# Performance work log

Measured on AMD Instinct MI355X. Metric: run time of the kernel, lower is better.

## Reference

```python
import jax, jax.numpy as jnp
import numpy as np
from functools import partial

ALPHA = 0.5
GAMMA = 0.01
BIG = 1e8  # boundary init, matches compute_softdtw (exp(-BIG/gamma)==0)


def pairwise_sq(x, y):
    # x: [N, d], y: [M, d] -> squared euclidean distances [N, M], clamped at 0
    xn = jnp.sum(x * x, axis=1)[:, None]
    yn = jnp.sum(y * y, axis=1)[None, :]
    d = xn + yn - 2.0 * (x @ y.T)
    return jnp.clip(d, 0.0, None)


def softdtw(D, gamma):
    # soft-DTW DP: V[i,j] = D[i-1,j-1] + softmin(V[i,j-1], V[i-1,j-1], V[i-1,j])
    # scan over rows; inner scan over columns (sequential dependence on V[i,j-1])
    N, M = D.shape

    def row_step(prev_row, d_row):
        # prev_row: V[i-1, 0..M]  (length M+1)
        def col_step(v_left, inp):
            d, v_diag, v_up = inp
            r = jnp.stack([v_left, v_diag, v_up]) * (-1.0 / gamma)
            v = d - gamma * jax.nn.logsumexp(r)  # stable soft-min
            return v, v

        _, row_vals = jax.lax.scan(
            col_step,
            jnp.asarray(BIG, D.dtype),                 # V[i, 0]
            (d_row, prev_row[:-1], prev_row[1:]),      # D[i-1,j-1], V[i-1,j-1], V[i-1,j]
        )
        new_row = jnp.concatenate([jnp.full((1,), BIG, D.dtype), row_vals])
        return new_row, None

    init_row = jnp.concatenate(
        [jnp.zeros((1,), D.dtype), jnp.full((M,), BIG, D.dtype)]
    )  # V[0, :] row with V[0,0]=0
    last_row, _ = jax.lax.scan(row_step, init_row, D)
    return last_row[-1]  # V[N, M]


def dilate_loss(y_pred, y_true, alpha=ALPHA, gamma=GAMMA):
    B, N = y_pred.shape[0], y_pred.shape[1]
    t = y_true.reshape(B, -1, 1)
    o = y_pred.reshape(B, -1, 1)
    D = jax.vmap(pairwise_sq)(t, o)  # [B, N, N]

    sd = partial(softdtw, gamma=gamma)
    # shape term: mean soft-DTW value over batch (SoftDTWBatch)
    loss_shape = jnp.mean(jax.vmap(sd)(D))
    # temporal term: E = d softDTW / d D (soft path), mean over batch (PathDTWBatch)
    path = jnp.mean(jax.vmap(jax.grad(sd))(D), axis=0)  # [N, N]
    idx = jnp.arange(1, N + 1, dtype=y_pred.dtype)
    omega = (idx[:, None] - idx[None, :]) ** 2  # pairwise_distances(range(1,N+1))
    loss_temporal = jnp.sum(path * omega) / (N * N)

    return alpha * loss_shape + (1.0 - alpha) * loss_temporal


def setup_inputs() -> dict:
    key = jax.random.key(0)
    k1, k2 = jax.random.split(key)
    B, N = 64, 256
    y_pred = jax.random.normal(k1, (B, N, 1), dtype=jnp.float32)
    y_true = jax.random.normal(k2, (B, N, 1), dtype=jnp.float32)
    return {"y_pred": y_pred, "y_true": y_true}


def reference(y_pred, y_true):
    return dilate_loss(y_pred, y_true)
```

## Files before the change

kernel.cpp:

```cpp
#include <hip/hip_runtime.h>

#define BATCH 64
#define NN 256
#define CSC   144.26950408889634f
#define RCSC  0.0069314718055994531f
#define BIGS  1.4426950408889634e10f


__device__ __forceinline__ float shr1(float x, float old) {
    return __int_as_float(__builtin_amdgcn_update_dpp(
        __float_as_int(old), __float_as_int(x), 0x138, 0xF, 0xF, false));
}

#define ITER(J, OINJ) {                                              \
    float sA = shr1(A, rdcA);                                        \
    float sU = shr1(U, rdcU);                                        \
    oc = shr1(oc, OINJ);                                             \
    rdcA = rdnA; rdcU = rdnU;                                        \
    float2 rr = ringr[((J) + 9) & 15];             \
    rdnA = rr.x; rdnU = rr.y;                                        \
    float m  = fminf(fminf(A, psA), sA);                             \
    float el = __builtin_amdgcn_exp2f(m - A);                        \
    float ed = __builtin_amdgcn_exp2f(m - psA);                      \
    float eu = __builtin_amdgcn_exp2f(m - sA);                       \
    float s  = el + ed + eu;                                         \
    float x  = T - oc;                                               \
    float nv = fmaf(CSC * x, x, m - __builtin_amdgcn_logf(s));       \
    float num = fmaf(el, U, fmaf(ed, psU, eu * sU));                 \
    float nt  = fmaf(num, __builtin_amdgcn_rcpf(s), dr * dr);        \
    if (l63) ringw[(J)] = make_float2(nv, nt);                       \
    psA = sA; psU = sU; A = nv; U = nt; dr -= 1.0f;                  \
}

__global__ __launch_bounds__(256) void dilate_fused(
    const float* __restrict__ y_pred,
    const float* __restrict__ y_true,
    float* __restrict__ out)
{
    const int b   = blockIdx.x;
    const int tid = threadIdx.x;
    const int w   = tid >> 6;
    const int l   = tid & 63;
    const bool l63 = (l == 63);

    __shared__ float  o_lds[1088];
    __shared__ float2 ring[5][16];

    const float4 z4 = make_float4(0.f, 0.f, 0.f, 0.f);
    if (tid < 128) ((float4*)o_lds)[tid] = z4;
    if (tid >= 128 && tid < 208) ((float4*)o_lds)[tid + 64] = z4;
    if (tid < 64) ((float4*)(o_lds + 512))[tid] =
        ((const float4*)(y_pred + b * NN))[tid];
    if (tid < 80) ((float2*)ring)[tid] = make_float2(BIGS, 0.f);

    const float T = y_true[b * NN + tid];
    __syncthreads();

    float A = BIGS, U = 0.f;
    float psA = (tid == 0) ? 0.f : BIGS;
    float psU = 0.f;
    float oc = 0.f;
    float dr = (float)(2 * tid + 8 * w);
    float rdcA = BIGS, rdcU = 0.f, rdnA = BIGS, rdnU = 0.f;

    float2* ringw = ring[w];
    const float2* ringr = ring[(w == 0) ? 4 : (w - 1)];
    const float4* o4 = ((const float4*)o_lds) + (128 - 18 * w);

    float4 fA = o4[0], fB = o4[1], fC = o4[2], fD = o4[3]; o4 += 4;

    #pragma unroll 1
    for (int blk = 0; blk < 33; ++blk) {
        float4 gA = o4[0], gB = o4[1], gC = o4[2], gD = o4[3]; o4 += 4;
        ITER(0,  fA.x) ITER(1,  fA.y) ITER(2,  fA.z) ITER(3,  fA.w)
        __syncthreads();
        ITER(4,  fB.x) ITER(5,  fB.y) ITER(6,  fB.z) ITER(7,  fB.w)
        __syncthreads();
        ITER(8,  fC.x) ITER(9,  fC.y) ITER(10, fC.z) ITER(11, fC.w)
        __syncthreads();
        ITER(12, fD.x) ITER(13, fD.y) ITER(14, fD.z) ITER(15, fD.w)
        __syncthreads();
        fA = gA; fB = gB; fC = gC; fD = gD;
    }
    ITER(0, fA.x) ITER(1, fA.y) ITER(2, fA.z) ITER(3, fA.w)
    ITER(4, fB.x) ITER(5, fB.y) ITER(6, fB.z)

    if (tid == 255) {
        float loss = 0.5f * (A * RCSC) * (1.0f / BATCH)
                   + 0.5f * U * (1.0f / ((float)BATCH * (float)(NN * NN)));
        atomicAdd(out, loss);
    }
}

extern "C" void kernel_launch(void* const* d_in, const int* in_sizes, int n_in,
                              void* d_out, int out_size, void* d_ws, size_t ws_size,
                              hipStream_t stream)
{
    const float* y_pred = (const float*)d_in[0];
    const float* y_true = (const float*)d_in[1];
    hipMemsetAsync(d_out, 0, sizeof(float), stream);
    dilate_fused<<<BATCH, 256, 0, stream>>>(y_pred, y_true, (float*)d_out);
}
```

Before: 97.85 us.

## Load per-lane pred values directly from LDS and defer ring writes by one step

Each lane now reads its own pred value straight from LDS with a lane-offset pointer. This replaces the DPP shift chain that passed values along the wave from a broadcast float4. The ring buffer is split into separate A and U float arrays, and the lane-63 write of each step is delayed to the next iteration so the store leaves the critical dependency chain. In exchange, every step issues per-lane LDS loads instead of one DPP op, and the correctness of the deferred-write timing against the read offset and barriers is not obvious.

```diff
diff --git a/kernel.cpp b/kernel.cpp
--- a/kernel.cpp
+++ b/kernel.cpp
@@ -12,13 +12,15 @@
         __float_as_int(old), __float_as_int(x), 0x138, 0xF, 0xF, false));
 }
 
-#define ITER(J, OINJ) {                                              \
+#define ITER(J) {                                                    \
+    if (l63) { ringwA[((J) + 15) & 15] = pnv;                        \
+               ringwU[((J) + 15) & 15] = pnt; }                      \
     float sA = shr1(A, rdcA);                                        \
     float sU = shr1(U, rdcU);                                        \
-    oc = shr1(oc, OINJ);                                             \
     rdcA = rdnA; rdcU = rdnU;                                        \
-    float2 rr = ringr[((J) + 9) & 15];             \
-    rdnA = rr.x; rdnU = rr.y;                                        \
+    rdnA = ringrA[((J) + 9) & 15];      \
+    rdnU = ringrU[((J) + 9) & 15];                                   \
+    float oc = o0; o0 = o1; o1 = opb[(J)];            \
     float m  = fminf(fminf(A, psA), sA);                             \
     float el = __builtin_amdgcn_exp2f(m - A);                        \
     float ed = __builtin_amdgcn_exp2f(m - psA);                      \
@@ -28,7 +30,7 @@
     float nv = fmaf(CSC * x, x, m - __builtin_amdgcn_logf(s));       \
     float num = fmaf(el, U, fmaf(ed, psU, eu * sU));                 \
     float nt  = fmaf(num, __builtin_amdgcn_rcpf(s), dr * dr);        \
-    if (l63) ringw[(J)] = make_float2(nv, nt);                       \
+    pnv = nv; pnt = nt;                                              \
     psA = sA; psU = sU; A = nv; U = nt; dr -= 1.0f;                  \
 }
 
@@ -43,15 +45,16 @@
     const int l   = tid & 63;
     const bool l63 = (l == 63);
 
-    __shared__ float  o_lds[1088];
-    __shared__ float2 ring[5][16];
+    __shared__ float o_lds[1088];
+    __shared__ float ringA[5][16];
+    __shared__ float ringU[5][16];
 
     const float4 z4 = make_float4(0.f, 0.f, 0.f, 0.f);
     if (tid < 128) ((float4*)o_lds)[tid] = z4;
     if (tid >= 128 && tid < 208) ((float4*)o_lds)[tid + 64] = z4;
     if (tid < 64) ((float4*)(o_lds + 512))[tid] =
         ((const float4*)(y_pred + b * NN))[tid];
-    if (tid < 80) ((float2*)ring)[tid] = make_float2(BIGS, 0.f);
+    if (tid < 80) { ((float*)ringA)[tid] = BIGS; ((float*)ringU)[tid] = 0.f; }
 
     const float T = y_true[b * NN + tid];
     __syncthreads();
@@ -59,31 +62,33 @@
     float A = BIGS, U = 0.f;
     float psA = (tid == 0) ? 0.f : BIGS;
     float psU = 0.f;
-    float oc = 0.f;
     float dr = (float)(2 * tid + 8 * w);
     float rdcA = BIGS, rdcU = 0.f, rdnA = BIGS, rdnU = 0.f;
+    float pnv = BIGS, pnt = 0.f;
 
-    float2* ringw = ring[w];
-    const float2* ringr = ring[(w == 0) ? 4 : (w - 1)];
-    const float4* o4 = ((const float4*)o_lds) + (128 - 18 * w);
+    float* ringwA = ringA[w];
+    float* ringwU = ringU[w];
+    const float* ringrA = ringA[(w == 0) ? 4 : (w - 1)];
+    const float* ringrU = ringU[(w == 0) ? 4 : (w - 1)];
 
-    float4 fA = o4[0], fB = o4[1], fC = o4[2], fD = o4[3]; o4 += 4;
+    const float* opb = o_lds + (512 - 72 * w - l);
+    float o0 = opb[0], o1 = opb[1];
+    opb += 2;
 
     #pragma unroll 1
     for (int blk = 0; blk < 33; ++blk) {
-        float4 gA = o4[0], gB = o4[1], gC = o4[2], gD = o4[3]; o4 += 4;
-        ITER(0,  fA.x) ITER(1,  fA.y) ITER(2,  fA.z) ITER(3,  fA.w)
+        ITER(0)  ITER(1)  ITER(2)  ITER(3)
         __syncthreads();
-        ITER(4,  fB.x) ITER(5,  fB.y) ITER(6,  fB.z) ITER(7,  fB.w)
+        ITER(4)  ITER(5)  ITER(6)  ITER(7)
         __syncthreads();
-        ITER(8,  fC.x) ITER(9,  fC.y) ITER(10, fC.z) ITER(11, fC.w)
+        ITER(8)  ITER(9)  ITER(10) ITER(11)
         __syncthreads();
-        ITER(12, fD.x) ITER(13, fD.y) ITER(14, fD.z) ITER(15, fD.w)
+        ITER(12) ITER(13) ITER(14) ITER(15)
         __syncthreads();
-        fA = gA; fB = gB; fC = gC; fD = gD;
+        opb += 16;
     }
-    ITER(0, fA.x) ITER(1, fA.y) ITER(2, fA.z) ITER(3, fA.w)
-    ITER(4, fB.x) ITER(5, fB.y) ITER(6, fB.z)
+    ITER(0) ITER(1) ITER(2) ITER(3)
+    ITER(4) ITER(5) ITER(6)
 
     if (tid == 255) {
         float loss = 0.5f * (A * RCSC) * (1.0f / BATCH)
```

Result: slower. 109.4 us (+11.8%).

## Halve barriers per block by widening inter-wave ring lag to eight steps

Applied to the files above, without the earlier changes.

Restructures the wavefront-pipelined soft-DTW so each wave reads its predecessor's boundary values through an 8-deep register queue, allowing one barrier every 8 column steps instead of every 4. The inter-wave skew grows (offsets 19 vs 18 per wave, more loop blocks, adjusted tail), trading extra pipeline fill steps for fewer __syncthreads. Aims to cut barrier stalls on the serial critical path, at the cost of more registers and a longer prologue/epilogue.

```diff
diff --git a/kernel.cpp b/kernel.cpp
--- a/kernel.cpp
+++ b/kernel.cpp
@@ -12,13 +12,10 @@
         __float_as_int(old), __float_as_int(x), 0x138, 0xF, 0xF, false));
 }
 
-#define ITER(J, OINJ) {                                              \
-    float sA = shr1(A, rdcA);                                        \
-    float sU = shr1(U, rdcU);                                        \
+#define ITER(J, OINJ, QV) {                                          \
+    float sA = shr1(A, (QV).x);                                      \
+    float sU = shr1(U, (QV).y);                                      \
     oc = shr1(oc, OINJ);                                             \
-    rdcA = rdnA; rdcU = rdnU;                                        \
-    float2 rr = ringr[((J) + 9) & 15];             \
-    rdnA = rr.x; rdnU = rr.y;                                        \
     float m  = fminf(fminf(A, psA), sA);                             \
     float el = __builtin_amdgcn_exp2f(m - A);                        \
     float ed = __builtin_amdgcn_exp2f(m - psA);                      \
@@ -31,6 +28,8 @@
     if (l63) ringw[(J)] = make_float2(nv, nt);                       \
     psA = sA; psU = sU; A = nv; U = nt; dr -= 1.0f;                  \
 }
+
+#define RD(J, QD) { QD = ringr[((J) + 8) & 15]; }
 
 __global__ __launch_bounds__(256) void dilate_fused(
     const float* __restrict__ y_pred,
@@ -60,30 +59,42 @@
     float psA = (tid == 0) ? 0.f : BIGS;
     float psU = 0.f;
     float oc = 0.f;
-    float dr = (float)(2 * tid + 8 * w);
-    float rdcA = BIGS, rdcU = 0.f, rdnA = BIGS, rdnU = 0.f;
+    float dr = (float)(2 * tid + 12 * w);
+    const float2 qi = make_float2(BIGS, 0.f);
+    float2 q0 = qi, q1 = qi, q2 = qi, q3 = qi, q4 = qi, q5 = qi, q6 = qi, q7 = qi;
 
     float2* ringw = ring[w];
     const float2* ringr = ring[(w == 0) ? 4 : (w - 1)];
-    const float4* o4 = ((const float4*)o_lds) + (128 - 18 * w);
+    const float4* o4 = ((const float4*)o_lds) + (128 - 19 * w);
 
     float4 fA = o4[0], fB = o4[1], fC = o4[2], fD = o4[3]; o4 += 4;
 
     #pragma unroll 1
-    for (int blk = 0; blk < 33; ++blk) {
+    for (int blk = 0; blk < 34; ++blk) {
         float4 gA = o4[0], gB = o4[1], gC = o4[2], gD = o4[3]; o4 += 4;
-        ITER(0,  fA.x) ITER(1,  fA.y) ITER(2,  fA.z) ITER(3,  fA.w)
+        ITER(0,  fA.x, q3) RD(0,  q0)
+        ITER(1,  fA.y, q4) RD(1,  q1)
+        ITER(2,  fA.z, q5) RD(2,  q2)
+        ITER(3,  fA.w, q6) RD(3,  q3)
+        ITER(4,  fB.x, q7) RD(4,  q4)
+        ITER(5,  fB.y, q0) RD(5,  q5)
+        ITER(6,  fB.z, q1) RD(6,  q6) RD(7, q7)
+        ITER(7,  fB.w, q2)
         __syncthreads();
-        ITER(4,  fB.x) ITER(5,  fB.y) ITER(6,  fB.z) ITER(7,  fB.w)
-        __syncthreads();
-        ITER(8,  fC.x) ITER(9,  fC.y) ITER(10, fC.z) ITER(11, fC.w)
-        __syncthreads();
-        ITER(12, fD.x) ITER(13, fD.y) ITER(14, fD.z) ITER(15, fD.w)
+        ITER(8,  fC.x, q3) RD(8,  q0)
+        ITER(9,  fC.y, q4) RD(9,  q1)
+        ITER(10, fC.z, q5) RD(10, q2)
+        ITER(11, fC.w, q6) RD(11, q3)
+        ITER(12, fD.x, q7) RD(12, q4)
+        ITER(13, fD.y, q0) RD(13, q5)
+        ITER(14, fD.z, q1) RD(14, q6) RD(15, q7)
+        ITER(15, fD.w, q2)
         __syncthreads();
         fA = gA; fB = gB; fC = gC; fD = gD;
     }
-    ITER(0, fA.x) ITER(1, fA.y) ITER(2, fA.z) ITER(3, fA.w)
-    ITER(4, fB.x) ITER(5, fB.y) ITER(6, fB.z)
+    ITER(0, fA.x, q3)
+    ITER(1, fA.y, q4)
+    ITER(2, fA.z, q5)
 
     if (tid == 255) {
         float loss = 0.5f * (A * RCSC) * (1.0f / BATCH)
```

Result: no change. 97.05 us (-0.8%).

## Halve barriers by packing two cells per ring slot and prescaling inputs

Applied to the files above, without the earlier changes.

The inter-wave ring buffer now stores two consecutive cells per float4 slot, so each wave hands off 8 cells per barrier instead of 4. The wave skew is widened and the main loop is restructured into 17 double-blocks with reloaded ring reads, which halves the number of __syncthreads per column sweep. Inputs are prescaled by sqrt of the log2 scale so the distance term drops a multiply, and min3 is done with one v_min3 instruction. The added skew lengthens the pipeline fill and drain, and the reworked indexing raises correctness risk.

```diff
diff --git a/kernel.cpp b/kernel.cpp
--- a/kernel.cpp
+++ b/kernel.cpp
@@ -4,6 +4,7 @@
 #define NN 256
 #define CSC   144.26950408889634f
 #define RCSC  0.0069314718055994531f
+#define SQC   12.011224079f
 #define BIGS  1.4426950408889634e10f
 
 
@@ -12,25 +13,34 @@
         __float_as_int(old), __float_as_int(x), 0x138, 0xF, 0xF, false));
 }
 
-#define ITER(J, OINJ) {                                              \
-    float sA = shr1(A, rdcA);                                        \
-    float sU = shr1(U, rdcU);                                        \
+__device__ __forceinline__ float min3f(float a, float b, float c) {
+    float d;
+    asm("v_min3_f32 %0, %1, %2, %3" : "=v"(d) : "v"(a), "v"(b), "v"(c));
+    return d;
+}
+
+#define CELLX(OINJ, QA, QB, PRE, POST) {                             \
+    float sA = shr1(A, QA);                                          \
+    float sU = shr1(U, QB);                                          \
     oc = shr1(oc, OINJ);                                             \
-    rdcA = rdnA; rdcU = rdnU;                                        \
-    float2 rr = ringr[((J) + 9) & 15];             \
-    rdnA = rr.x; rdnU = rr.y;                                        \
-    float m  = fminf(fminf(A, psA), sA);                             \
+    PRE                                                              \
+    float m  = min3f(A, psA, sA);                                    \
     float el = __builtin_amdgcn_exp2f(m - A);                        \
     float ed = __builtin_amdgcn_exp2f(m - psA);                      \
     float eu = __builtin_amdgcn_exp2f(m - sA);                       \
     float s  = el + ed + eu;                                         \
     float x  = T - oc;                                               \
-    float nv = fmaf(CSC * x, x, m - __builtin_amdgcn_logf(s));       \
+    float nv = fmaf(x, x, m - __builtin_amdgcn_logf(s));             \
     float num = fmaf(el, U, fmaf(ed, psU, eu * sU));                 \
     float nt  = fmaf(num, __builtin_amdgcn_rcpf(s), dr * dr);        \
-    if (l63) ringw[(J)] = make_float2(nv, nt);                       \
+    POST                                                             \
     psA = sA; psU = sU; A = nv; U = nt; dr -= 1.0f;                  \
 }
+
+#define CELL(OINJ, QA, QB) CELLX(OINJ, QA, QB, , )
+#define CELL_W(OINJ, QA, QB, SLOT)                                   \
+    CELLX(OINJ, QA, QB, float wv = A; float wu = U;,                 \
+          if (l63) ringw[SLOT] = make_float4(wv, wu, nv, nt);)
 
 __global__ __launch_bounds__(256) void dilate_fused(
     const float* __restrict__ y_pred,
@@ -44,46 +54,80 @@
     const bool l63 = (l == 63);
 
     __shared__ float  o_lds[1088];
-    __shared__ float2 ring[5][16];
+    __shared__ float4 ring[5][8];
 
     const float4 z4 = make_float4(0.f, 0.f, 0.f, 0.f);
     if (tid < 128) ((float4*)o_lds)[tid] = z4;
     if (tid >= 128 && tid < 208) ((float4*)o_lds)[tid + 64] = z4;
-    if (tid < 64) ((float4*)(o_lds + 512))[tid] =
-        ((const float4*)(y_pred + b * NN))[tid];
-    if (tid < 80) ((float2*)ring)[tid] = make_float2(BIGS, 0.f);
+    if (tid < 64) {
+        float4 ov = ((const float4*)(y_pred + b * NN))[tid];
+        ov.x *= SQC; ov.y *= SQC; ov.z *= SQC; ov.w *= SQC;
+        ((float4*)(o_lds + 512))[tid] = ov;
+    }
+    if (tid < 40) ((float4*)ring)[tid] = make_float4(BIGS, 0.f, BIGS, 0.f);
 
-    const float T = y_true[b * NN + tid];
+    const float T = y_true[b * NN + tid] * SQC;
     __syncthreads();
 
     float A = BIGS, U = 0.f;
     float psA = (tid == 0) ? 0.f : BIGS;
     float psU = 0.f;
     float oc = 0.f;
-    float dr = (float)(2 * tid + 8 * w);
-    float rdcA = BIGS, rdcU = 0.f, rdnA = BIGS, rdnU = 0.f;
+    float dr = (float)(2 * tid + 12 * w);
+    const float4 qi = make_float4(BIGS, 0.f, BIGS, 0.f);
+    float4 q0 = qi, q1 = qi, q2 = qi, q3 = qi;
 
-    float2* ringw = ring[w];
-    const float2* ringr = ring[(w == 0) ? 4 : (w - 1)];
-    const float4* o4 = ((const float4*)o_lds) + (128 - 18 * w);
+    float4* ringw = ring[w];
+    const float4* ringr = ring[(w == 0) ? 4 : (w - 1)];
+    const float4* o4 = ((const float4*)o_lds) + (128 - 19 * w);
 
     float4 fA = o4[0], fB = o4[1], fC = o4[2], fD = o4[3]; o4 += 4;
+    float4 gA, gB, gC, gD;
 
     #pragma unroll 1
-    for (int blk = 0; blk < 33; ++blk) {
-        float4 gA = o4[0], gB = o4[1], gC = o4[2], gD = o4[3]; o4 += 4;
-        ITER(0,  fA.x) ITER(1,  fA.y) ITER(2,  fA.z) ITER(3,  fA.w)
+    for (int blk = 0; blk < 17; ++blk) {
+        gA = o4[0]; gB = o4[1]; gC = o4[2]; gD = o4[3];
+        q0 = ringr[4]; CELL  (fA.x, q1.z, q1.w)
+                       CELL_W(fA.y, q2.x, q2.y, 0)
+        q1 = ringr[5]; CELL  (fA.z, q2.z, q2.w)
+                       CELL_W(fA.w, q3.x, q3.y, 1)
+        q2 = ringr[6]; CELL  (fB.x, q3.z, q3.w)
+                       CELL_W(fB.y, q0.x, q0.y, 2)
+        q3 = ringr[7]; CELL  (fB.z, q0.z, q0.w)
+                       CELL_W(fB.w, q1.x, q1.y, 3)
         __syncthreads();
-        ITER(4,  fB.x) ITER(5,  fB.y) ITER(6,  fB.z) ITER(7,  fB.w)
+        q0 = ringr[0]; CELL  (fC.x, q1.z, q1.w)
+                       CELL_W(fC.y, q2.x, q2.y, 4)
+        q1 = ringr[1]; CELL  (fC.z, q2.z, q2.w)
+                       CELL_W(fC.w, q3.x, q3.y, 5)
+        q2 = ringr[2]; CELL  (fD.x, q3.z, q3.w)
+                       CELL_W(fD.y, q0.x, q0.y, 6)
+        q3 = ringr[3]; CELL  (fD.z, q0.z, q0.w)
+                       CELL_W(fD.w, q1.x, q1.y, 7)
         __syncthreads();
-        ITER(8,  fC.x) ITER(9,  fC.y) ITER(10, fC.z) ITER(11, fC.w)
+        fA = o4[4]; fB = o4[5]; fC = o4[6]; fD = o4[7]; o4 += 8;
+        q0 = ringr[4]; CELL  (gA.x, q1.z, q1.w)
+                       CELL_W(gA.y, q2.x, q2.y, 0)
+        q1 = ringr[5]; CELL  (gA.z, q2.z, q2.w)
+                       CELL_W(gA.w, q3.x, q3.y, 1)
+        q2 = ringr[6]; CELL  (gB.x, q3.z, q3.w)
+                       CELL_W(gB.y, q0.x, q0.y, 2)
+        q3 = ringr[7]; CELL  (gB.z, q0.z, q0.w)
+                       CELL_W(gB.w, q1.x, q1.y, 3)
         __syncthreads();
-        ITER(12, fD.x) ITER(13, fD.y) ITER(14, fD.z) ITER(15, fD.w)
+        q0 = ringr[0]; CELL  (gC.x, q1.z, q1.w)
+                       CELL_W(gC.y, q2.x, q2.y, 4)
+        q1 = ringr[1]; CELL  (gC.z, q2.z, q2.w)
+                       CELL_W(gC.w, q3.x, q3.y, 5)
+        q2 = ringr[2]; CELL  (gD.x, q3.z, q3.w)
+                       CELL_W(gD.y, q0.x, q0.y, 6)
+        q3 = ringr[3]; CELL  (gD.z, q0.z, q0.w)
+                       CELL_W(gD.w, q1.x, q1.y, 7)
         __syncthreads();
-        fA = gA; fB = gB; fC = gC; fD = gD;
     }
-    ITER(0, fA.x) ITER(1, fA.y) ITER(2, fA.z) ITER(3, fA.w)
-    ITER(4, fB.x) ITER(5, fB.y) ITER(6, fB.z)
+    CELL(fA.x, q1.z, q1.w)
+    CELL(fA.y, q2.x, q2.y)
+    CELL(fA.z, q2.z, q2.w)
 
     if (tid == 255) {
         float loss = 0.5f * (A * RCSC) * (1.0f / BATCH)
```

New measurement: 94.86 us, median of 2. 3.1% less time.
